# Kernel tuning notes

Measured on AMD Instinct MI355X. Metric: run time of the kernel, lower is better.

## Reference

```python
import jax, jax.numpy as jnp
import numpy as np

T = 400      # timestamps (window length chosen == timestamps -> no padding branch)
D = 10000    # out_dimension (HDC hypervector dim)
TWO_PI = 2.0 * np.pi


def setup_inputs() -> dict:
    key = jax.random.key(0)
    ks = jax.random.split(key, 10)
    # monotonically increasing timestamps so jerk dt > 0
    t = jnp.cumsum(jax.random.uniform(ks[0], (T,), jnp.float32) + 0.5)
    xyz = jax.random.normal(ks[1], (T, 3), jnp.float32)
    inp = jnp.concatenate([t[:, None], xyz], axis=1)  # [T,4] = (t, x, y, z)
    W1 = jax.random.normal(ks[2], (D, T * 3), jnp.float32)
    b1 = jax.random.uniform(ks[3], (D,), jnp.float32, 0.0, TWO_PI)
    W2 = jax.random.normal(ks[4], (D, T * 3), jnp.float32)
    b2 = jax.random.uniform(ks[5], (D,), jnp.float32, 0.0, TWO_PI)
    W3 = jax.random.normal(ks[6], (D, T * 2), jnp.float32)
    b3 = jax.random.uniform(ks[7], (D,), jnp.float32, 0.0, TWO_PI)
    W4 = jax.random.normal(ks[8], (D, 3), jnp.float32)
    b4 = jax.random.uniform(ks[9], (D,), jnp.float32, 0.0, TWO_PI)
    return {"input": inp, "W1": W1, "b1": b1, "W2": W2, "b2": b2,
            "W3": W3, "b3": b3, "W4": W4, "b4": b4}


def _hypertangent(x, W, b):
    # HyperTangent random-feature embedding: tanh(W @ x + b)
    return jnp.tanh(W @ x + b)


def reference(input, W1, b1, W2, b2, W3, b3, W4, b4):
    t = input[:, 0] - input[0, 0]           # zero-base the time column
    xyz = input[:, 1:]                      # [T,3]
    sq = xyz * xyz
    mags = jnp.sqrt(jnp.sum(sq, axis=1))    # [T]
    energy = jnp.sum(sq, axis=0) / xyz.shape[0]  # [3]
    # vectorized jerk: (x_{i+1}-x_i)/(t_{i+1}-t_i), with a leading zeros row
    dt = (t[1:] - t[:-1])[:, None]          # [T-1,1]
    jerks = jnp.concatenate(
        [jnp.zeros((1, 3), input.dtype), (xyz[1:] - xyz[:-1]) / dt], axis=0)  # [T,3]
    jerk_mags = jnp.sqrt(jnp.sum(jerks * jerks, axis=1))  # [T]
    # window == timestamps -> no padding path
    features1 = jnp.concatenate([xyz[:, 0], xyz[:, 1], xyz[:, 2]])      # [3T]
    features2 = jnp.concatenate([jerks[:, 0], jerks[:, 1], jerks[:, 2]])  # [3T]
    features3 = jnp.concatenate([mags, jerk_mags])                       # [2T]
    hv1 = _hypertangent(features1, W1, b1)
    hv2 = _hypertangent(features2, W2, b2)
    hv3 = _hypertangent(features3, W3, b3)
    hv4 = _hypertangent(energy, W4, b4)
    return jnp.tanh(hv1 * hv4 + hv2 + hv3)  # [D]
```

## Files before the change

kernel.cpp:

```cpp
#include <hip/hip_runtime.h>
#include <hip/hip_bf16.h>
#include <math.h>

#define T_PTS 400
#define D_OUT 10000
#define L12   1200
#define L3    800
#define ROW   3200
#define FEAT_TOTAL (ROW + 3)

__global__ __launch_bounds__(512)
void hdc_features_kernel(const float* __restrict__ in, float* __restrict__ feat) {
    __shared__ float red[3][8];
    const int tid = threadIdx.x;
    float ex = 0.f, ey = 0.f, ez = 0.f;

    if (tid < T_PTS) {
        const float4 cur = reinterpret_cast<const float4*>(in)[tid];
        const float x = cur.y, y = cur.z, z = cur.w;
        feat[tid]        = x;
        feat[400 + tid]  = y;
        feat[800 + tid]  = z;
        feat[2400 + tid] = sqrtf(x * x + y * y + z * z);
        ex = x * x; ey = y * y; ez = z * z;

        float jx = 0.f, jy = 0.f, jz = 0.f;
        if (tid > 0) {
            const float4 prev = reinterpret_cast<const float4*>(in)[tid - 1];
            const float dt = cur.x - prev.x;
            const float inv = 1.0f / dt;
            jx = (x - prev.y) * inv;
            jy = (y - prev.z) * inv;
            jz = (z - prev.w) * inv;
        }
        feat[1200 + tid] = jx;
        feat[1600 + tid] = jy;
        feat[2000 + tid] = jz;
        feat[2800 + tid] = sqrtf(jx * jx + jy * jy + jz * jz);
    }

    #pragma unroll
    for (int off = 32; off; off >>= 1) {
        ex += __shfl_down(ex, off, 64);
        ey += __shfl_down(ey, off, 64);
        ez += __shfl_down(ez, off, 64);
    }
    const int wave = tid >> 6, lane = tid & 63;
    if (lane == 0) { red[0][wave] = ex; red[1][wave] = ey; red[2][wave] = ez; }
    __syncthreads();
    if (tid == 0) {
        float sx = 0.f, sy = 0.f, sz = 0.f;
        #pragma unroll
        for (int w = 0; w < 8; ++w) { sx += red[0][w]; sy += red[1][w]; sz += red[2][w]; }
        const float invT = 1.0f / (float)T_PTS;
        feat[3200] = sx * invT;
        feat[3201] = sy * invT;
        feat[3202] = sz * invT;
    }
}

__global__ __launch_bounds__(256)
void hdc_gemv_kernel(const float* __restrict__ W1, const float* __restrict__ b1,
                     const float* __restrict__ W2, const float* __restrict__ b2,
                     const float* __restrict__ W3, const float* __restrict__ b3,
                     const float* __restrict__ W4, const float* __restrict__ b4,
                     const float* __restrict__ feat, float* __restrict__ out) {
    __shared__ __align__(16) float g[FEAT_TOTAL];
    const int tid = threadIdx.x;
    const int wave = tid >> 6, lane = tid & 63;
    const int d = blockIdx.x * 4 + wave;
    const int c0 = lane * 4;

    const float* __restrict__ w1 = W1 + (size_t)d * L12;
    const float* __restrict__ w2 = W2 + (size_t)d * L12;
    const float* __restrict__ w3 = W3 + (size_t)d * L3;

    float4 r[12];
    #pragma unroll
    for (int i = 0; i < 12; ++i) {
        const int k = 256 * i + c0;
        const float* p;
        if (i < 4)       p = w1 + k;
        else if (i == 4) p = (k < L12) ? (w1 + k) : (w2 + (k - L12));
        else if (i < 9)  p = w2 + (k - L12);
        else if (i == 9) p = (k < 2400) ? (w2 + (k - L12)) : (w3 + (k - 2400));
        else             p = w3 + (k - 2400);
        r[i] = *reinterpret_cast<const float4*>(p);
    }
    const float2 rt = *reinterpret_cast<const float2*>(w3 + (3072 - 2400) + 2 * lane);

    {
        float4* g4 = reinterpret_cast<float4*>(g);
        const float4* feat4 = reinterpret_cast<const float4*>(feat);
        for (int i = tid; i < ROW / 4; i += 256) g4[i] = feat4[i];
        if (tid == 0) { g[3200] = feat[3200]; g[3201] = feat[3201]; g[3202] = feat[3202]; }
    }
    __syncthreads();

    float acc1 = 0.f, acc2 = 0.f, acc3 = 0.f;
    #pragma unroll
    for (int i = 0; i < 12; ++i) {
        const int k = 256 * i + c0;
        const float4 s = *reinterpret_cast<const float4*>(&g[k]);
        const float t = r[i].x * s.x + r[i].y * s.y + r[i].z * s.z + r[i].w * s.w;
        if (i < 4)       acc1 += t;
        else if (i == 4) { acc1 += (k < L12) ? t : 0.f; acc2 += (k < L12) ? 0.f : t; }
        else if (i < 9)  acc2 += t;
        else if (i == 9) { acc2 += (k < 2400) ? t : 0.f; acc3 += (k < 2400) ? 0.f : t; }
        else             acc3 += t;
    }
    {
        const int k = 3072 + 2 * lane;
        acc3 += rt.x * g[k] + rt.y * g[k + 1];
    }

    float bb1 = 0.f, bb2 = 0.f, bb3 = 0.f, bb4 = 0.f, w40 = 0.f, w41 = 0.f, w42 = 0.f;
    if (lane == 0) {
        bb1 = b1[d]; bb2 = b2[d]; bb3 = b3[d]; bb4 = b4[d];
        w40 = W4[(size_t)d * 3 + 0];
        w41 = W4[(size_t)d * 3 + 1];
        w42 = W4[(size_t)d * 3 + 2];
    }

    #pragma unroll
    for (int off = 32; off; off >>= 1) {
        acc1 += __shfl_down(acc1, off, 64);
        acc2 += __shfl_down(acc2, off, 64);
        acc3 += __shfl_down(acc3, off, 64);
    }

    if (lane == 0) {
        const float e0 = g[3200], e1 = g[3201], e2 = g[3202];
        const float hv1 = tanhf(acc1 + bb1);
        const float hv2 = tanhf(acc2 + bb2);
        const float hv3 = tanhf(acc3 + bb3);
        const float hv4 = tanhf(w40 * e0 + w41 * e1 + w42 * e2 + bb4);
        out[d] = tanhf(hv1 * hv4 + hv2 + hv3);
    }
}

extern "C" void kernel_launch(void* const* d_in, const int* in_sizes, int n_in,
                              void* d_out, int out_size, void* d_ws, size_t ws_size,
                              hipStream_t stream) {
    const float* input = (const float*)d_in[0];
    const float* W1 = (const float*)d_in[1];
    const float* b1 = (const float*)d_in[2];
    const float* W2 = (const float*)d_in[3];
    const float* b2 = (const float*)d_in[4];
    const float* W3 = (const float*)d_in[5];
    const float* b3 = (const float*)d_in[6];
    const float* W4 = (const float*)d_in[7];
    const float* b4 = (const float*)d_in[8];
    float* out = (float*)d_out;
    float* feat = (float*)d_ws;

    hdc_features_kernel<<<1, 512, 0, stream>>>(input, feat);
    hdc_gemv_kernel<<<D_OUT / 4, 256, 0, stream>>>(W1, b1, W2, b2, W3, b3,
                                                   W4, b4, feat, out);
}
```

Measured before the change: 163.8 us.

## Process four rows per wave with register-cached features and prefetched next row

Each wave now handles four output rows spaced 2500 apart, with 1250 blocks of 128 threads instead of 2500 blocks of 256. The feature vector sits in registers rather than shared memory, which removes the LDS staging and the block barrier. The next row's weights are loaded before the current row's reduction so memory latency overlaps compute. In exchange it uses more registers and launches fewer waves, which may lower occupancy for a bandwidth-bound GEMV.

```diff
diff --git a/kernel.cpp b/kernel.cpp
--- a/kernel.cpp
+++ b/kernel.cpp
@@ -7,7 +7,6 @@
 #define L12   1200
 #define L3    800
 #define ROW   3200
-#define FEAT_TOTAL (ROW + 3)
 
 __global__ __launch_bounds__(512)
 void hdc_features_kernel(const float* __restrict__ in, float* __restrict__ feat) {
@@ -59,82 +58,90 @@
     }
 }
 
-__global__ __launch_bounds__(256)
+#define LOAD_ROW()                                                            \
+    do {                                                                      \
+        _Pragma("unroll")                                                     \
+        for (int i = 0; i < 12; ++i) {                                        \
+            const int k = 256 * i + c0;                                       \
+            const float* p;                                                   \
+            if (i < 4)       p = w1 + k;                                      \
+            else if (i == 4) p = (k < L12) ? (w1 + k) : (w2 + (k - L12));     \
+            else if (i < 9)  p = w2 + (k - L12);                              \
+            else if (i == 9) p = (k < 2400) ? (w2 + (k - L12))                \
+                                            : (w3 + (k - 2400));              \
+            else             p = w3 + (k - 2400);                             \
+            r[i] = *reinterpret_cast<const float4*>(p);                       \
+        }                                                                     \
+        rt = *reinterpret_cast<const float2*>(w3 + 672 + 2 * lane);           \
+    } while (0)
+
+__global__ __launch_bounds__(128)
 void hdc_gemv_kernel(const float* __restrict__ W1, const float* __restrict__ b1,
                      const float* __restrict__ W2, const float* __restrict__ b2,
                      const float* __restrict__ W3, const float* __restrict__ b3,
                      const float* __restrict__ W4, const float* __restrict__ b4,
                      const float* __restrict__ feat, float* __restrict__ out) {
-    __shared__ __align__(16) float g[FEAT_TOTAL];
     const int tid = threadIdx.x;
     const int wave = tid >> 6, lane = tid & 63;
-    const int d = blockIdx.x * 4 + wave;
+    const int g = blockIdx.x * 2 + wave;
     const int c0 = lane * 4;
 
-    const float* __restrict__ w1 = W1 + (size_t)d * L12;
-    const float* __restrict__ w2 = W2 + (size_t)d * L12;
-    const float* __restrict__ w3 = W3 + (size_t)d * L3;
+    float4 s[12];
+    #pragma unroll
+    for (int i = 0; i < 12; ++i)
+        s[i] = *reinterpret_cast<const float4*>(feat + 256 * i + c0);
+    const float2 st = *reinterpret_cast<const float2*>(feat + 3072 + 2 * lane);
+
+    const float* __restrict__ w1 = W1 + (size_t)g * L12;
+    const float* __restrict__ w2 = W2 + (size_t)g * L12;
+    const float* __restrict__ w3 = W3 + (size_t)g * L3;
 
     float4 r[12];
-    #pragma unroll
-    for (int i = 0; i < 12; ++i) {
-        const int k = 256 * i + c0;
-        const float* p;
-        if (i < 4)       p = w1 + k;
-        else if (i == 4) p = (k < L12) ? (w1 + k) : (w2 + (k - L12));
-        else if (i < 9)  p = w2 + (k - L12);
-        else if (i == 9) p = (k < 2400) ? (w2 + (k - L12)) : (w3 + (k - 2400));
-        else             p = w3 + (k - 2400);
-        r[i] = *reinterpret_cast<const float4*>(p);
-    }
-    const float2 rt = *reinterpret_cast<const float2*>(w3 + (3072 - 2400) + 2 * lane);
+    float2 rt;
+    LOAD_ROW();
 
-    {
-        float4* g4 = reinterpret_cast<float4*>(g);
-        const float4* feat4 = reinterpret_cast<const float4*>(feat);
-        for (int i = tid; i < ROW / 4; i += 256) g4[i] = feat4[i];
-        if (tid == 0) { g[3200] = feat[3200]; g[3201] = feat[3201]; g[3202] = feat[3202]; }
-    }
-    __syncthreads();
+    float k1 = 0.f, k2 = 0.f, k3 = 0.f;
 
-    float acc1 = 0.f, acc2 = 0.f, acc3 = 0.f;
-    #pragma unroll
-    for (int i = 0; i < 12; ++i) {
-        const int k = 256 * i + c0;
-        const float4 s = *reinterpret_cast<const float4*>(&g[k]);
-        const float t = r[i].x * s.x + r[i].y * s.y + r[i].z * s.z + r[i].w * s.w;
-        if (i < 4)       acc1 += t;
-        else if (i == 4) { acc1 += (k < L12) ? t : 0.f; acc2 += (k < L12) ? 0.f : t; }
-        else if (i < 9)  acc2 += t;
-        else if (i == 9) { acc2 += (k < 2400) ? t : 0.f; acc3 += (k < 2400) ? 0.f : t; }
-        else             acc3 += t;
-    }
-    {
-        const int k = 3072 + 2 * lane;
-        acc3 += rt.x * g[k] + rt.y * g[k + 1];
+    for (int rr = 0; rr < 4; ++rr) {
+        float a1 = 0.f, a2 = 0.f, a3 = 0.f;
+        #pragma unroll
+        for (int i = 0; i < 12; ++i) {
+            const int k = 256 * i + c0;
+            const float t = r[i].x * s[i].x + r[i].y * s[i].y +
+                            r[i].z * s[i].z + r[i].w * s[i].w;
+            if (i < 4)       a1 += t;
+            else if (i == 4) { a1 += (k < L12) ? t : 0.f; a2 += (k < L12) ? 0.f : t; }
+            else if (i < 9)  a2 += t;
+            else if (i == 9) { a2 += (k < 2400) ? t : 0.f; a3 += (k < 2400) ? 0.f : t; }
+            else             a3 += t;
+        }
+        a3 += rt.x * st.x + rt.y * st.y;
+
+        if (rr < 3) {
+            w1 += (size_t)2500 * L12;
+            w2 += (size_t)2500 * L12;
+            w3 += (size_t)2500 * L3;
+            LOAD_ROW();
+        }
+
+        #pragma unroll
+        for (int off = 32; off; off >>= 1) {
+            a1 += __shfl_xor(a1, off, 64);
+            a2 += __shfl_xor(a2, off, 64);
+            a3 += __shfl_xor(a3, off, 64);
+        }
+        if (lane == rr) { k1 = a1; k2 = a2; k3 = a3; }
     }
 
-    float bb1 = 0.f, bb2 = 0.f, bb3 = 0.f, bb4 = 0.f, w40 = 0.f, w41 = 0.f, w42 = 0.f;
-    if (lane == 0) {
-        bb1 = b1[d]; bb2 = b2[d]; bb3 = b3[d]; bb4 = b4[d];
-        w40 = W4[(size_t)d * 3 + 0];
-        w41 = W4[(size_t)d * 3 + 1];
-        w42 = W4[(size_t)d * 3 + 2];
-    }
-
-    #pragma unroll
-    for (int off = 32; off; off >>= 1) {
-        acc1 += __shfl_down(acc1, off, 64);
-        acc2 += __shfl_down(acc2, off, 64);
-        acc3 += __shfl_down(acc3, off, 64);
-    }
-
-    if (lane == 0) {
-        const float e0 = g[3200], e1 = g[3201], e2 = g[3202];
-        const float hv1 = tanhf(acc1 + bb1);
-        const float hv2 = tanhf(acc2 + bb2);
-        const float hv3 = tanhf(acc3 + bb3);
-        const float hv4 = tanhf(w40 * e0 + w41 * e1 + w42 * e2 + bb4);
+    if (lane < 4) {
+        const int d = g + lane * 2500;
+        const float e0 = feat[3200], e1 = feat[3201], e2 = feat[3202];
+        const float hv1 = tanhf(k1 + b1[d]);
+        const float hv2 = tanhf(k2 + b2[d]);
+        const float hv3 = tanhf(k3 + b3[d]);
+        const float hv4 = tanhf(W4[(size_t)d * 3 + 0] * e0 +
+                                W4[(size_t)d * 3 + 1] * e1 +
+                                W4[(size_t)d * 3 + 2] * e2 + b4[d]);
         out[d] = tanhf(hv1 * hv4 + hv2 + hv3);
     }
 }
@@ -155,6 +162,6 @@
     float* feat = (float*)d_ws;
 
     hdc_features_kernel<<<1, 512, 0, stream>>>(input, feat);
-    hdc_gemv_kernel<<<D_OUT / 4, 256, 0, stream>>>(W1, b1, W2, b2, W3, b3,
-                                                   W4, b4, feat, out);
+    hdc_gemv_kernel<<<1250, 128, 0, stream>>>(W1, b1, W2, b2, W3, b3,
+                                              W4, b4, feat, out);
 }
```

Result: no change. 165.0 us (+0.8%).

## Split GEMV into per-chunk wave dot kernel plus separate tanh combine kernel

Applied to the files above, without the earlier changes.

Replaces the one-wave-per-row GEMV with a kernel in which each wave computes a single 256-element chunk dot product, writing partial sums to workspace. A second kernel reduces the partials and applies the tanh combination. The aim is more memory-level parallelism and finer load balancing for streaming the 128 MB of weights. The cost is an extra launch, a partial-sum round trip, and 140k tiny waves that each issue only one load. The old path is kept as a fallback when workspace is too small.

```diff
diff --git a/kernel.cpp b/kernel.cpp
--- a/kernel.cpp
+++ b/kernel.cpp
@@ -6,8 +6,10 @@
 #define D_OUT 10000
 #define L12   1200
 #define L3    800
-#define ROW   3200
-#define FEAT_TOTAL (ROW + 3)
+
+#define FEAT_F 3328
+#define PART_OFF 3328
+#define WS_NEED ((FEAT_F + 16 * D_OUT) * sizeof(float))
 
 __global__ __launch_bounds__(512)
 void hdc_features_kernel(const float* __restrict__ in, float* __restrict__ feat) {
@@ -60,12 +62,65 @@
 }
 
 __global__ __launch_bounds__(256)
-void hdc_gemv_kernel(const float* __restrict__ W1, const float* __restrict__ b1,
-                     const float* __restrict__ W2, const float* __restrict__ b2,
-                     const float* __restrict__ W3, const float* __restrict__ b3,
-                     const float* __restrict__ W4, const float* __restrict__ b4,
-                     const float* __restrict__ feat, float* __restrict__ out) {
-    __shared__ __align__(16) float g[FEAT_TOTAL];
+void hdc_dot_kernel(const float* __restrict__ W1, const float* __restrict__ W2,
+                    const float* __restrict__ W3, const float* __restrict__ feat,
+                    float* __restrict__ partial) {
+    const int wid = blockIdx.x * 4 + (threadIdx.x >> 6);
+    const int lane = threadIdx.x & 63;
+
+    const float* __restrict__ Wm;
+    int row, c, len, foff, slot;
+    if (wid < 50000) {
+        Wm = W1; row = wid / 5; c = wid - row * 5; len = L12; foff = 0; slot = c;
+    } else if (wid < 100000) {
+        const int u = wid - 50000;
+        Wm = W2; row = u / 5; c = u - row * 5; len = L12; foff = 1200; slot = 5 + c;
+    } else {
+        const int u = wid - 100000;
+        Wm = W3; row = u / 4; c = u - row * 4; len = L3; foff = 2400; slot = 10 + c;
+    }
+
+    const int k = c * 256 + lane * 4;
+    float t = 0.f;
+    if (k < len) {
+        const float4 w = *reinterpret_cast<const float4*>(Wm + (size_t)row * len + k);
+        const float4 f = *reinterpret_cast<const float4*>(feat + foff + k);
+        t = w.x * f.x + w.y * f.y + w.z * f.z + w.w * f.w;
+    }
+    #pragma unroll
+    for (int off = 32; off; off >>= 1) t += __shfl_down(t, off, 64);
+    if (lane == 0) partial[row * 16 + slot] = t;
+}
+
+__global__ __launch_bounds__(256)
+void hdc_tanh_kernel(const float* __restrict__ partial,
+                     const float* __restrict__ b1, const float* __restrict__ b2,
+                     const float* __restrict__ b3, const float* __restrict__ W4,
+                     const float* __restrict__ b4, const float* __restrict__ feat,
+                     float* __restrict__ out) {
+    const int d = blockIdx.x * 256 + threadIdx.x;
+    if (d >= D_OUT) return;
+    const float* __restrict__ p = partial + d * 16;
+    const float a1 = ((p[0] + p[1]) + (p[2] + p[3])) + p[4];
+    const float a2 = ((p[5] + p[6]) + (p[7] + p[8])) + p[9];
+    const float a3 = (p[10] + p[11]) + (p[12] + p[13]);
+    const float e0 = feat[3200], e1 = feat[3201], e2 = feat[3202];
+    const float hv1 = tanhf(a1 + b1[d]);
+    const float hv2 = tanhf(a2 + b2[d]);
+    const float hv3 = tanhf(a3 + b3[d]);
+    const float hv4 = tanhf(W4[(size_t)d * 3 + 0] * e0 +
+                            W4[(size_t)d * 3 + 1] * e1 +
+                            W4[(size_t)d * 3 + 2] * e2 + b4[d]);
+    out[d] = tanhf(hv1 * hv4 + hv2 + hv3);
+}
+
+__global__ __launch_bounds__(256)
+void hdc_gemv_fallback(const float* __restrict__ W1, const float* __restrict__ b1,
+                       const float* __restrict__ W2, const float* __restrict__ b2,
+                       const float* __restrict__ W3, const float* __restrict__ b3,
+                       const float* __restrict__ W4, const float* __restrict__ b4,
+                       const float* __restrict__ feat, float* __restrict__ out) {
+    __shared__ __align__(16) float g[3203];
     const int tid = threadIdx.x;
     const int wave = tid >> 6, lane = tid & 63;
     const int d = blockIdx.x * 4 + wave;
@@ -87,12 +142,12 @@
         else             p = w3 + (k - 2400);
         r[i] = *reinterpret_cast<const float4*>(p);
     }
-    const float2 rt = *reinterpret_cast<const float2*>(w3 + (3072 - 2400) + 2 * lane);
+    const float2 rt = *reinterpret_cast<const float2*>(w3 + 672 + 2 * lane);
 
     {
         float4* g4 = reinterpret_cast<float4*>(g);
         const float4* feat4 = reinterpret_cast<const float4*>(feat);
-        for (int i = tid; i < ROW / 4; i += 256) g4[i] = feat4[i];
+        for (int i = tid; i < 800; i += 256) g4[i] = feat4[i];
         if (tid == 0) { g[3200] = feat[3200]; g[3201] = feat[3201]; g[3202] = feat[3202]; }
     }
     __syncthreads();
@@ -114,14 +169,6 @@
         acc3 += rt.x * g[k] + rt.y * g[k + 1];
     }
 
-    float bb1 = 0.f, bb2 = 0.f, bb3 = 0.f, bb4 = 0.f, w40 = 0.f, w41 = 0.f, w42 = 0.f;
-    if (lane == 0) {
-        bb1 = b1[d]; bb2 = b2[d]; bb3 = b3[d]; bb4 = b4[d];
-        w40 = W4[(size_t)d * 3 + 0];
-        w41 = W4[(size_t)d * 3 + 1];
-        w42 = W4[(size_t)d * 3 + 2];
-    }
-
     #pragma unroll
     for (int off = 32; off; off >>= 1) {
         acc1 += __shfl_down(acc1, off, 64);
@@ -131,10 +178,12 @@
 
     if (lane == 0) {
         const float e0 = g[3200], e1 = g[3201], e2 = g[3202];
-        const float hv1 = tanhf(acc1 + bb1);
-        const float hv2 = tanhf(acc2 + bb2);
-        const float hv3 = tanhf(acc3 + bb3);
-        const float hv4 = tanhf(w40 * e0 + w41 * e1 + w42 * e2 + bb4);
+        const float hv1 = tanhf(acc1 + b1[d]);
+        const float hv2 = tanhf(acc2 + b2[d]);
+        const float hv3 = tanhf(acc3 + b3[d]);
+        const float hv4 = tanhf(W4[(size_t)d * 3 + 0] * e0 +
+                                W4[(size_t)d * 3 + 1] * e1 +
+                                W4[(size_t)d * 3 + 2] * e2 + b4[d]);
         out[d] = tanhf(hv1 * hv4 + hv2 + hv3);
     }
 }
@@ -155,6 +204,14 @@
     float* feat = (float*)d_ws;
 
     hdc_features_kernel<<<1, 512, 0, stream>>>(input, feat);
-    hdc_gemv_kernel<<<D_OUT / 4, 256, 0, stream>>>(W1, b1, W2, b2, W3, b3,
-                                                   W4, b4, feat, out);
-}
+
+    if (ws_size >= WS_NEED) {
+        float* partial = feat + PART_OFF;
+        hdc_dot_kernel<<<35000, 256, 0, stream>>>(W1, W2, W3, feat, partial);
+        hdc_tanh_kernel<<<(D_OUT + 255) / 256, 256, 0, stream>>>(
+            partial, b1, b2, b3, W4, b4, feat, out);
+    } else {
+        hdc_gemv_fallback<<<D_OUT / 4, 256, 0, stream>>>(W1, b1, W2, b2, W3, b3,
+                                                         W4, b4, feat, out);
+    }
+}
```

After: 164.7 us. About the same (+0.5%).
